# Kernel tuning notes

Hardware: AMD Instinct MI355X
Metric: run time of the kernel (lower is better)

## Reference

```python
import jax, jax.numpy as jnp
import numpy as np

IN, H, OUT, FC_H = 8, 128, 4, 64
BN_EPS = 1e-5


def _lstm_cell(x, h, c, Wih, Whh, bih, bhh):
    # PyTorch gate order: i, f, g, o
    z = x @ Wih.T + h @ Whh.T + (bih + bhh)  # [B, 4H]
    i, f, g, o = jnp.split(z, 4, axis=-1)
    i, f, o = jax.nn.sigmoid(i), jax.nn.sigmoid(f), jax.nn.sigmoid(o)
    g = jnp.tanh(g)
    c = f * c + i * g
    h = o * jnp.tanh(c)
    return h, c


def setup_inputs() -> dict:
    key = jax.random.key(0)
    ks = jax.random.split(key, 20)
    s = 0.05
    inp = {
        "x": jax.random.normal(ks[0], (4096, 512, IN), jnp.float32),
        # LSTM layer 0 (input_size -> H)
        "Wih0": jax.random.normal(ks[1], (4 * H, IN), jnp.float32) * s,
        "Whh0": jax.random.normal(ks[2], (4 * H, H), jnp.float32) * s,
        "bih0": jax.random.normal(ks[3], (4 * H,), jnp.float32) * s,
        "bhh0": jax.random.normal(ks[4], (4 * H,), jnp.float32) * s,
        # LSTM layer 1 (H -> H)
        "Wih1": jax.random.normal(ks[5], (4 * H, H), jnp.float32) * s,
        "Whh1": jax.random.normal(ks[6], (4 * H, H), jnp.float32) * s,
        "bih1": jax.random.normal(ks[7], (4 * H,), jnp.float32) * s,
        "bhh1": jax.random.normal(ks[8], (4 * H,), jnp.float32) * s,
        # BatchNorm1d(H) in eval mode: affine params + running stats
        "bn_gamma": jnp.ones((H,), jnp.float32),
        "bn_beta": jnp.zeros((H,), jnp.float32),
        "bn_mean": jax.random.normal(ks[9], (H,), jnp.float32) * s,
        "bn_var": jax.random.uniform(ks[10], (H,), jnp.float32, 0.5, 1.5),
        # fc: Linear(H, 64) -> ReLU -> Linear(64, OUT)
        "W1": jax.random.normal(ks[11], (FC_H, H), jnp.float32) * s,
        "b1": jax.random.normal(ks[12], (FC_H,), jnp.float32) * s,
        "W2": jax.random.normal(ks[13], (OUT, FC_H), jnp.float32) * s,
        "b2": jax.random.normal(ks[14], (OUT,), jnp.float32) * s,
        # feedback: Linear(OUT, IN)
        "Wf": jax.random.normal(ks[15], (IN, OUT), jnp.float32) * s,
        "bf": jax.random.normal(ks[16], (IN,), jnp.float32) * s,
        "prediction_steps": 64,
    }
    return inp


def reference(x, Wih0, Whh0, bih0, bhh0, Wih1, Whh1, bih1, bhh1,
              bn_gamma, bn_beta, bn_mean, bn_var, W1, b1, W2, b2, Wf, bf,
              prediction_steps):
    B = x.shape[0]
    h0 = jnp.zeros((B, H), x.dtype)
    state0 = (h0, h0, h0, h0)  # (h_l0, c_l0, h_l1, c_l1)

    def step(state, xt):
        hl0, cl0, hl1, cl1 = state
        hl0, cl0 = _lstm_cell(xt, hl0, cl0, Wih0, Whh0, bih0, bhh0)
        hl1, cl1 = _lstm_cell(hl0, hl1, cl1, Wih1, Whh1, bih1, bhh1)
        return (hl0, cl0, hl1, cl1), None

    # Encoding pass over the full sequence (seq_len=1 per step in torch loop)
    xs = jnp.swapaxes(x, 0, 1)  # [T, B, IN]
    state, _ = jax.lax.scan(step, state0, xs)

    def fc(h):
        hn = (h - bn_mean) * jax.lax.rsqrt(bn_var + BN_EPS) * bn_gamma + bn_beta
        return jax.nn.relu(hn @ W1.T + b1) @ W2.T + b2

    def dec_step(carry, _):
        hl0, cl0, hl1, cl1, xin = carry
        hl0, cl0 = _lstm_cell(xin, hl0, cl0, Wih0, Whh0, bih0, bhh0)
        hl1, cl1 = _lstm_cell(hl0, hl1, cl1, Wih1, Whh1, bih1, bhh1)
        out = fc(hl1)                 # [B, OUT]
        xin = out @ Wf.T + bf         # feedback -> next input [B, IN]
        return (hl0, cl0, hl1, cl1, xin), out

    carry0 = (*state, x[:, -1, :])
    _, outs = jax.lax.scan(dec_step, carry0, None, length=prediction_steps)
    return jnp.swapaxes(outs, 0, 1)  # [B, prediction_steps, OUT]
```

## Files before the change

kernel.cpp:

```cpp
#include <hip/hip_runtime.h>

#define THREADS 512
#define BT 16
#define TLEN 512
#define HD 128
#define NT 4
#define WSTR 132
#define HSTR 136

#define SC_IFO (-1.4426950408889634f)
#define SC_G   ( 2.8853900817779268f)

typedef __attribute__((ext_vector_type(8))) short bf16x8;
typedef __attribute__((ext_vector_type(4))) float f32x4;

__device__ __forceinline__ short f2bf(float f) {
  unsigned u = __float_as_uint(f);
  u += 0x7fff + ((u >> 16) & 1);
  return (short)(u >> 16);
}

__device__ __forceinline__ unsigned cvt_pk_bf16(float lo, float hi) {
  unsigned r;
  asm("v_cvt_pk_bf16_f32 %0, %1, %2" : "=v"(r) : "v"(lo), "v"(hi));
  return r;
}

__device__ __forceinline__ bf16x8 pack8(f32x4 a, f32x4 b) {
  bf16x8 r;
  r[0]=f2bf(a[0]); r[1]=f2bf(a[1]); r[2]=f2bf(a[2]); r[3]=f2bf(a[3]);
  r[4]=f2bf(b[0]); r[5]=f2bf(b[1]); r[6]=f2bf(b[2]); r[7]=f2bf(b[3]);
  return r;
}
__device__ __forceinline__ bf16x8 load8s(const float* p, float s) {
  const f32x4* q4 = (const f32x4*)p;
  return pack8(q4[0] * s, q4[1] * s);
}

__global__ __launch_bounds__(THREADS, 2) void lstm_kernel(
    const float* __restrict__ xg,
    const float* __restrict__ Wih0, const float* __restrict__ Whh0,
    const float* __restrict__ bih0, const float* __restrict__ bhh0,
    const float* __restrict__ Wih1, const float* __restrict__ Whh1,
    const float* __restrict__ bih1, const float* __restrict__ bhh1,
    const float* __restrict__ gma, const float* __restrict__ bta,
    const float* __restrict__ mu,  const float* __restrict__ var,
    const float* __restrict__ W1,  const float* __restrict__ b1,
    const float* __restrict__ W2,  const float* __restrict__ b2,
    const float* __restrict__ Wf,  const float* __restrict__ bfv,
    const int* __restrict__ psP,
    float* __restrict__ dout)
{
  __shared__ __align__(16) short WhhL[512*WSTR];
  __shared__ __align__(16) short h0A[2][BT*HSTR];
  __shared__ __align__(16) short h1A[2][BT*HSTR];
  __shared__ __align__(16) short xA[2][BT*32];
  __shared__ float a1L[64*BT];
  __shared__ float W2L[4*65];
  __shared__ float WcL[8*68];
  __shared__ float bcL[8];
  __shared__ float b2L[4];
  __shared__ float b1cL[64];
  __shared__ float sLs[HD];

  const int tid = threadIdx.x;
  const int w   = tid >> 6;
  const int l   = tid & 63;
  const int ln  = l & 15;
  const int q   = l >> 4;
  const int gb0 = blockIdx.x * BT;
  const int ps  = psP[0];

  for (int i = tid; i < BT*32; i += THREADS) { xA[0][i] = 0; xA[1][i] = 0; }
  for (int i = tid; i < BT*HSTR; i += THREADS) {
    h0A[0][i] = 0; h0A[1][i] = 0; h1A[0][i] = 0; h1A[1][i] = 0;
  }
  if (tid < BT) {
    xA[0][tid*32 + 8] = (short)0x3F80;
    xA[1][tid*32 + 8] = (short)0x3F80;
  }
  if (tid < HD) sLs[tid] = gma[tid] * rsqrtf(var[tid] + 1e-5f);
  if (tid < 260) { int o = tid / 65, p = tid % 65; W2L[tid] = (p < 64) ? W2[o*64 + p] : 0.f; }
  {
    int i0 = tid >> 6, p = tid & 63;
    float acc = 0.f;
    #pragma unroll
    for (int o = 0; o < 4; o++) acc += Wf[i0*4 + o] * W2[o*64 + p];
    WcL[i0*68 + p] = acc;
  }
  if (tid < 8) {
    float acc = bfv[tid];
    #pragma unroll
    for (int o = 0; o < 4; o++) acc += Wf[tid*4 + o] * b2[o];
    bcL[tid] = acc;
  }
  if (tid < 4)  b2L[tid] = b2[tid];
  for (int i = tid; i < 512*HD; i += THREADS) {
    int og = i >> 7, k = i & 127;
    float sc = ((og >> 7) == 2) ? SC_G : SC_IFO;
    WhhL[og*WSTR + k] = f2bf(Whh0[i] * sc);
  }

  bf16x8 wih0f[NT], wih1f[NT][4], whh1f[NT][4];
  float b1sum[NT];
  #pragma unroll
  for (int nt = 0; nt < NT; nt++) {
    int og = nt*HD + (w << 4) + ln;
    const float sc = (nt == 2) ? SC_G : SC_IFO;
    {
      bf16x8 r;
      #pragma unroll
      for (int j = 0; j < 8; j++) {
        int k = q*8 + j;
        float v = 0.f;
        if (k < 8) v = Wih0[og*8 + k];
        else if (k == 8) v = bih0[og] + bhh0[og];
        r[j] = f2bf(v * sc);
      }
      wih0f[nt] = r;
    }
    #pragma unroll
    for (int kk = 0; kk < 4; kk++) {
      int k0 = kk*32 + q*8;
      wih1f[nt][kk] = load8s(Wih1 + og*HD + k0, sc);
      whh1f[nt][kk] = load8s(Whh1 + og*HD + k0, sc);
    }
    b1sum[nt] = (bih1[og] + bhh1[og]) * sc;
  }
  __syncthreads();

  if (tid < 64) {
    float acc = b1[tid];
    for (int j = 0; j < HD; j++)
      acc += (bta[j] - mu[j]*sLs[j]) * W1[tid*HD + j];
    b1cL[tid] = acc;
  }
  if (tid < 128) {
    const int b = tid >> 3, i2 = tid & 7;
    xA[0][b*32 + i2] = f2bf(xg[(size_t)(gb0 + b)*(TLEN*8) + i2]);
  }
  __syncthreads();

  f32x4 c0s = {0.f,0.f,0.f,0.f};
  f32x4 c1s = {0.f,0.f,0.f,0.f};

  const int aoffX = ln*32   + q*8;
  const int aoffH = ln*HSTR + q*8;
  const int hwoff = (q*4)*HSTR + (w<<4) + ln;

  auto gates = [&](const f32x4& gi, const f32x4& gf, const f32x4& gg, const f32x4& go,
                   f32x4& cs, short* hw) {
    float hv[4];
    #pragma unroll
    for (int r = 0; r < 4; r++) {
      float ei = __builtin_amdgcn_exp2f(gi[r]);
      float ef = __builtin_amdgcn_exp2f(gf[r]);
      float eg = __builtin_amdgcn_exp2f(gg[r]);
      float eo = __builtin_amdgcn_exp2f(go[r]);
      float f   = __builtin_amdgcn_rcpf(1.0f + ef);
      float rig = __builtin_amdgcn_rcpf((1.0f + ei) * (1.0f + eg));
      float igs = (SC_G * eg - SC_G) * rig;
      float c   = f * cs[r] + igs;
      cs[r] = c;
      float ec  = __builtin_amdgcn_exp2f(c);
      float roc = __builtin_amdgcn_rcpf((1.0f + eo) * (1.0f + ec));
      hv[r] = (ec - 1.0f) * roc;
    }
    unsigned p01 = cvt_pk_bf16(hv[0], hv[1]);
    unsigned p23 = cvt_pk_bf16(hv[2], hv[3]);
    hw[0*HSTR] = (short)p01;
    hw[1*HSTR] = (short)(p01 >> 16);
    hw[2*HSTR] = (short)p23;
    hw[3*HSTR] = (short)(p23 >> 16);
  };

  auto layer0 = [&](const short* xr, const bf16x8* ah, short* h0w) {
    bf16x8 ax = *(const bf16x8*)(xr + aoffX);
    f32x4 ac[NT];
    #pragma unroll
    for (int nt = 0; nt < NT; nt++) {
      const int cb = (nt*HD + (w<<4) + ln)*WSTR + q*8;
      f32x4 a = {0.f,0.f,0.f,0.f};
      a = __builtin_amdgcn_mfma_f32_16x16x32_bf16(ax, wih0f[nt], a, 0, 0, 0);
      #pragma unroll
      for (int kk = 0; kk < 4; kk++) {
        bf16x8 wb = *(const bf16x8*)(WhhL + cb + kk*32);
        a = __builtin_amdgcn_mfma_f32_16x16x32_bf16(ah[kk], wb, a, 0, 0, 0);
      }
      ac[nt] = a;
    }
    gates(ac[0], ac[1], ac[2], ac[3], c0s, h0w + hwoff);
  };

  auto layer1 = [&](const bf16x8* ah, const short* h1r, short* h1w) {
    bf16x8 a1k[4];
    #pragma unroll
    for (int kk = 0; kk < 4; kk++)
      a1k[kk] = *(const bf16x8*)(h1r + aoffH + kk*32);
    f32x4 ac[NT];
    #pragma unroll
    for (int nt = 0; nt < NT; nt++) {
      f32x4 a; a[0]=a[1]=a[2]=a[3]=b1sum[nt];
      #pragma unroll
      for (int kk = 0; kk < 4; kk++) {
        a = __builtin_amdgcn_mfma_f32_16x16x32_bf16(ah[kk],  wih1f[nt][kk], a, 0, 0, 0);
        a = __builtin_amdgcn_mfma_f32_16x16x32_bf16(a1k[kk], whh1f[nt][kk], a, 0, 0, 0);
      }
      ac[nt] = a;
    }
    gates(ac[0], ac[1], ac[2], ac[3], c1s, h1w + hwoff);
  };

  auto enc_iter = [&](int k, const short* xr, short* xw,
                      const short* h0r, short* h0w,
                      const short* h1r, short* h1w, bool doL0, bool doL1) {
    const int b = tid >> 3, i2 = tid & 7;
    const bool pf = doL0 && (k + 1 < TLEN) && (tid < 128);
    float xp = 0.f;
    if (pf) xp = xg[(size_t)(gb0 + b)*(TLEN*8) + (size_t)(k+1)*8 + i2];
    bf16x8 ah[4];
    #pragma unroll
    for (int kk = 0; kk < 4; kk++)
      ah[kk] = *(const bf16x8*)(h0r + aoffH + kk*32);
    bf16x8 a1k[4];
    if (doL1) {
      #pragma unroll
      for (int kk = 0; kk < 4; kk++)
        a1k[kk] = *(const bf16x8*)(h1r + aoffH + kk*32);
    }
    f32x4 ac0[NT], ac1[NT];
    if (doL0) {
      bf16x8 ax = *(const bf16x8*)(xr + aoffX);
      #pragma unroll
      for (int nt = 0; nt < NT; nt++) {
        const int cb = (nt*HD + (w<<4) + ln)*WSTR + q*8;
        f32x4 a = {0.f,0.f,0.f,0.f};
        a = __builtin_amdgcn_mfma_f32_16x16x32_bf16(ax, wih0f[nt], a, 0, 0, 0);
        #pragma unroll
        for (int kk = 0; kk < 4; kk++) {
          bf16x8 wb = *(const bf16x8*)(WhhL + cb + kk*32);
          a = __builtin_amdgcn_mfma_f32_16x16x32_bf16(ah[kk], wb, a, 0, 0, 0);
        }
        ac0[nt] = a;
      }
    }
    if (doL1) {
      #pragma unroll
      for (int nt = 0; nt < NT; nt++) {
        f32x4 a; a[0]=a[1]=a[2]=a[3]=b1sum[nt];
        #pragma unroll
        for (int kk = 0; kk < 4; kk++) {
          a = __builtin_amdgcn_mfma_f32_16x16x32_bf16(ah[kk],  wih1f[nt][kk], a, 0, 0, 0);
          a = __builtin_amdgcn_mfma_f32_16x16x32_bf16(a1k[kk], whh1f[nt][kk], a, 0, 0, 0);
        }
        ac1[nt] = a;
      }
    }
    if (doL0) gates(ac0[0], ac0[1], ac0[2], ac0[3], c0s, h0w + hwoff);
    if (doL1) gates(ac1[0], ac1[1], ac1[2], ac1[3], c1s, h1w + hwoff);
    if (pf) xw[b*32 + i2] = f2bf(xp);
    __syncthreads();
  };

  enc_iter(0, xA[0], xA[1], h0A[1], h0A[0], h1A[0], h1A[1], true, false);
  enc_iter(1, xA[1], xA[0], h0A[0], h0A[1], h1A[1], h1A[0], true, true);
  for (int k = 2; k < TLEN; k += 2) {
    enc_iter(k,     xA[0], xA[1], h0A[1], h0A[0], h1A[0], h1A[1], true, true);
    enc_iter(k + 1, xA[1], xA[0], h0A[0], h0A[1], h1A[1], h1A[0], true, true);
  }
  enc_iter(TLEN, xA[0], xA[1], h0A[1], h0A[0], h1A[0], h1A[1], false, true);

  bf16x8 w1f[4];
  #pragma unroll
  for (int kk = 0; kk < 4; kk++) {
    bf16x8 r;
    if (w < 4) {
      int p = w*16 + ln;
      #pragma unroll
      for (int j = 0; j < 8; j++) {
        int k = kk*32 + q*8 + j;
        r[j] = f2bf(sLs[k] * W1[p*HD + k]);
      }
    } else {
      #pragma unroll
      for (int j = 0; j < 8; j++) r[j] = 0;
    }
    w1f[kk] = r;
  }

  for (int s = 0; s < ps; s++) {
    int rb = (s & 1) ^ 1;
    __syncthreads();
    {
      bf16x8 ah[4];
      #pragma unroll
      for (int kk = 0; kk < 4; kk++)
        ah[kk] = *(const bf16x8*)(h0A[rb] + aoffH + kk*32);
      layer0(xA[1], ah, h0A[rb^1]);
    }
    __syncthreads();
    {
      bf16x8 ah[4];
      #pragma unroll
      for (int kk = 0; kk < 4; kk++)
        ah[kk] = *(const bf16x8*)(h0A[rb^1] + aoffH + kk*32);
      layer1(ah, h1A[rb], h1A[rb^1]);
    }
    const short* h1n = h1A[rb^1];
    __syncthreads();
    if (w < 4) {
      f32x4 aa = {0.f,0.f,0.f,0.f};
      #pragma unroll
      for (int kk = 0; kk < 4; kk++) {
        bf16x8 ahn = *(const bf16x8*)(h1n + aoffH + kk*32);
        aa = __builtin_amdgcn_mfma_f32_16x16x32_bf16(ahn, w1f[kk], aa, 0, 0, 0);
      }
      float bb = b1cL[w*16 + ln];
      #pragma unroll
      for (int r = 0; r < 4; r++)
        a1L[(w*16 + ln)*16 + q*4 + r] = fmaxf(aa[r] + bb, 0.f);
    }
    __syncthreads();
    if (tid < 128) {
      int b = tid >> 3, i2 = tid & 7;
      float v = bcL[i2];
      for (int p = 0; p < 64; p++)
        v += a1L[p*16 + b] * WcL[i2*68 + p];
      xA[1][b*32 + i2] = f2bf(v);
    } else if (tid < 192) {
      int t = tid - 128, b = t & 15, o = t >> 4;
      float acc2 = b2L[o];
      for (int p = 0; p < 64; p++)
        acc2 += a1L[p*16 + b] * W2L[o*65 + p];
      dout[(size_t)(gb0 + b)*(ps*4) + s*4 + o] = acc2;
    }
  }
}

extern "C" void kernel_launch(void* const* d_in, const int* in_sizes, int n_in,
                              void* d_out, int out_size, void* d_ws, size_t ws_size,
                              hipStream_t stream) {
  (void)in_sizes; (void)n_in; (void)d_ws; (void)ws_size; (void)out_size;
  lstm_kernel<<<dim3(4096/BT), dim3(THREADS), 0, stream>>>(
      (const float*)d_in[0],  (const float*)d_in[1],  (const float*)d_in[2],
      (const float*)d_in[3],  (const float*)d_in[4],  (const float*)d_in[5],
      (const float*)d_in[6],  (const float*)d_in[7],  (const float*)d_in[8],
      (const float*)d_in[9],  (const float*)d_in[10], (const float*)d_in[11],
      (const float*)d_in[12], (const float*)d_in[13], (const float*)d_in[14],
      (const float*)d_in[15], (const float*)d_in[16], (const float*)d_in[17],
      (const float*)d_in[18], (const int*)d_in[19],   (float*)d_out);
}
```

Baseline: 1.266 ms.

## Software-pipeline encoder so layer-0 gates overlap layer-1 MFMAs with single-buffered state

Restructures the encoder loop so each step issues layer-1 MFMAs for the previous step while computing layer-0 gates, then issues next-step layer-0 MFMAs while computing layer-1 gates, with two barriers per step. Hidden states move from double buffers to single buffers in shared memory, x is prefetched two steps ahead, and the decoder buffer indexing is adjusted to match. The aim is to hide MFMA latency behind transcendental gate math. The cost is an extra barrier per step and more live registers, which could lower occupancy.

```diff
diff --git a/kernel.cpp b/kernel.cpp
--- a/kernel.cpp
+++ b/kernel.cpp
@@ -137,7 +137,8 @@
   }
   if (tid < 128) {
     const int b = tid >> 3, i2 = tid & 7;
-    xA[0][b*32 + i2] = f2bf(xg[(size_t)(gb0 + b)*(TLEN*8) + i2]);
+    xA[0][b*32 + i2] = f2bf(xg[(size_t)(gb0 + b)*(TLEN*8) + 0*8 + i2]);
+    xA[1][b*32 + i2] = f2bf(xg[(size_t)(gb0 + b)*(TLEN*8) + 1*8 + i2]);
   }
   __syncthreads();
 
@@ -174,9 +175,8 @@
     hw[3*HSTR] = (short)(p23 >> 16);
   };
 
-  auto layer0 = [&](const short* xr, const bf16x8* ah, short* h0w) {
+  auto issueL0 = [&](const bf16x8* ahv, const short* xr, f32x4* acc) {
     bf16x8 ax = *(const bf16x8*)(xr + aoffX);
-    f32x4 ac[NT];
     #pragma unroll
     for (int nt = 0; nt < NT; nt++) {
       const int cb = (nt*HD + (w<<4) + ln)*WSTR + q*8;
@@ -185,90 +185,70 @@
       #pragma unroll
       for (int kk = 0; kk < 4; kk++) {
         bf16x8 wb = *(const bf16x8*)(WhhL + cb + kk*32);
-        a = __builtin_amdgcn_mfma_f32_16x16x32_bf16(ah[kk], wb, a, 0, 0, 0);
-      }
-      ac[nt] = a;
-    }
-    gates(ac[0], ac[1], ac[2], ac[3], c0s, h0w + hwoff);
-  };
-
-  auto layer1 = [&](const bf16x8* ah, const short* h1r, short* h1w) {
-    bf16x8 a1k[4];
-    #pragma unroll
-    for (int kk = 0; kk < 4; kk++)
-      a1k[kk] = *(const bf16x8*)(h1r + aoffH + kk*32);
-    f32x4 ac[NT];
+        a = __builtin_amdgcn_mfma_f32_16x16x32_bf16(ahv[kk], wb, a, 0, 0, 0);
+      }
+      acc[nt] = a;
+    }
+  };
+  auto issueL1 = [&](const bf16x8* ahv, const bf16x8* a1v, f32x4* acc) {
     #pragma unroll
     for (int nt = 0; nt < NT; nt++) {
       f32x4 a; a[0]=a[1]=a[2]=a[3]=b1sum[nt];
       #pragma unroll
       for (int kk = 0; kk < 4; kk++) {
-        a = __builtin_amdgcn_mfma_f32_16x16x32_bf16(ah[kk],  wih1f[nt][kk], a, 0, 0, 0);
-        a = __builtin_amdgcn_mfma_f32_16x16x32_bf16(a1k[kk], whh1f[nt][kk], a, 0, 0, 0);
-      }
-      ac[nt] = a;
-    }
-    gates(ac[0], ac[1], ac[2], ac[3], c1s, h1w + hwoff);
-  };
-
-  auto enc_iter = [&](int k, const short* xr, short* xw,
-                      const short* h0r, short* h0w,
-                      const short* h1r, short* h1w, bool doL0, bool doL1) {
+        a = __builtin_amdgcn_mfma_f32_16x16x32_bf16(ahv[kk], wih1f[nt][kk], a, 0, 0, 0);
+        a = __builtin_amdgcn_mfma_f32_16x16x32_bf16(a1v[kk], whh1f[nt][kk], a, 0, 0, 0);
+      }
+      acc[nt] = a;
+    }
+  };
+
+  bf16x8 ahp[4];
+  f32x4 ac0[NT];
+  #pragma unroll
+  for (int kk = 0; kk < 4; kk++)
+    ahp[kk] = *(const bf16x8*)(h0A[0] + aoffH + kk*32);
+  issueL0(ahp, xA[0], ac0);
+  __syncthreads();
+
+  for (int k = 0; k < TLEN; ++k) {
+    const bool dL1  = (k >= 1);
+    const bool dL0n = (k + 1 < TLEN);
+    const bool dX   = (k + 2 < TLEN) && (tid < 128);
     const int b = tid >> 3, i2 = tid & 7;
-    const bool pf = doL0 && (k + 1 < TLEN) && (tid < 128);
     float xp = 0.f;
-    if (pf) xp = xg[(size_t)(gb0 + b)*(TLEN*8) + (size_t)(k+1)*8 + i2];
+    if (dX) xp = xg[(size_t)(gb0 + b)*(TLEN*8) + (size_t)(k+2)*8 + i2];
+    f32x4 ac1[NT];
+    if (dL1) {
+      bf16x8 a1k[4];
+      #pragma unroll
+      for (int kk = 0; kk < 4; kk++)
+        a1k[kk] = *(const bf16x8*)(h1A[0] + aoffH + kk*32);
+      issueL1(ahp, a1k, ac1);
+    }
+    gates(ac0[0], ac0[1], ac0[2], ac0[3], c0s, h0A[0] + hwoff);
+    __syncthreads();
     bf16x8 ah[4];
     #pragma unroll
     for (int kk = 0; kk < 4; kk++)
-      ah[kk] = *(const bf16x8*)(h0r + aoffH + kk*32);
+      ah[kk] = *(const bf16x8*)(h0A[0] + aoffH + kk*32);
+    if (dX) xA[k & 1][b*32 + i2] = f2bf(xp);
+    if (dL0n) issueL0(ah, xA[(k + 1) & 1], ac0);
+    if (dL1) gates(ac1[0], ac1[1], ac1[2], ac1[3], c1s, h1A[0] + hwoff);
+    __syncthreads();
+    #pragma unroll
+    for (int kk = 0; kk < 4; kk++) ahp[kk] = ah[kk];
+  }
+  {
     bf16x8 a1k[4];
-    if (doL1) {
-      #pragma unroll
-      for (int kk = 0; kk < 4; kk++)
-        a1k[kk] = *(const bf16x8*)(h1r + aoffH + kk*32);
-    }
-    f32x4 ac0[NT], ac1[NT];
-    if (doL0) {
-      bf16x8 ax = *(const bf16x8*)(xr + aoffX);
-      #pragma unroll
-      for (int nt = 0; nt < NT; nt++) {
-        const int cb = (nt*HD + (w<<4) + ln)*WSTR + q*8;
-        f32x4 a = {0.f,0.f,0.f,0.f};
-        a = __builtin_amdgcn_mfma_f32_16x16x32_bf16(ax, wih0f[nt], a, 0, 0, 0);
-        #pragma unroll
-        for (int kk = 0; kk < 4; kk++) {
-          bf16x8 wb = *(const bf16x8*)(WhhL + cb + kk*32);
-          a = __builtin_amdgcn_mfma_f32_16x16x32_bf16(ah[kk], wb, a, 0, 0, 0);
-        }
-        ac0[nt] = a;
-      }
-    }
-    if (doL1) {
-      #pragma unroll
-      for (int nt = 0; nt < NT; nt++) {
-        f32x4 a; a[0]=a[1]=a[2]=a[3]=b1sum[nt];
-        #pragma unroll
-        for (int kk = 0; kk < 4; kk++) {
-          a = __builtin_amdgcn_mfma_f32_16x16x32_bf16(ah[kk],  wih1f[nt][kk], a, 0, 0, 0);
-          a = __builtin_amdgcn_mfma_f32_16x16x32_bf16(a1k[kk], whh1f[nt][kk], a, 0, 0, 0);
-        }
-        ac1[nt] = a;
-      }
-    }
-    if (doL0) gates(ac0[0], ac0[1], ac0[2], ac0[3], c0s, h0w + hwoff);
-    if (doL1) gates(ac1[0], ac1[1], ac1[2], ac1[3], c1s, h1w + hwoff);
-    if (pf) xw[b*32 + i2] = f2bf(xp);
-    __syncthreads();
-  };
-
-  enc_iter(0, xA[0], xA[1], h0A[1], h0A[0], h1A[0], h1A[1], true, false);
-  enc_iter(1, xA[1], xA[0], h0A[0], h0A[1], h1A[1], h1A[0], true, true);
-  for (int k = 2; k < TLEN; k += 2) {
-    enc_iter(k,     xA[0], xA[1], h0A[1], h0A[0], h1A[0], h1A[1], true, true);
-    enc_iter(k + 1, xA[1], xA[0], h0A[0], h0A[1], h1A[1], h1A[0], true, true);
-  }
-  enc_iter(TLEN, xA[0], xA[1], h0A[1], h0A[0], h1A[0], h1A[1], false, true);
+    #pragma unroll
+    for (int kk = 0; kk < 4; kk++)
+      a1k[kk] = *(const bf16x8*)(h1A[0] + aoffH + kk*32);
+    f32x4 ac1[NT];
+    issueL1(ahp, a1k, ac1);
+    __syncthreads();
+    gates(ac1[0], ac1[1], ac1[2], ac1[3], c1s, h1A[0] + hwoff);
+  }
 
   bf16x8 w1f[4];
   #pragma unroll
@@ -288,8 +268,23 @@
     w1f[kk] = r;
   }
 
+  auto layer0 = [&](const short* xr, const bf16x8* ahv, short* h0w) {
+    f32x4 ac[NT];
+    issueL0(ahv, xr, ac);
+    gates(ac[0], ac[1], ac[2], ac[3], c0s, h0w + hwoff);
+  };
+  auto layer1 = [&](const bf16x8* ahv, const short* h1r, short* h1w) {
+    bf16x8 a1k[4];
+    #pragma unroll
+    for (int kk = 0; kk < 4; kk++)
+      a1k[kk] = *(const bf16x8*)(h1r + aoffH + kk*32);
+    f32x4 ac[NT];
+    issueL1(ahv, a1k, ac);
+    gates(ac[0], ac[1], ac[2], ac[3], c1s, h1w + hwoff);
+  };
+
   for (int s = 0; s < ps; s++) {
-    int rb = (s & 1) ^ 1;
+    int rb = s & 1;
     __syncthreads();
     {
       bf16x8 ah[4];
```

Result: slower. 1.320 ms (+4.3%).
